# Kernel tuning notes

Measured on AMD Instinct MI355X. Metric: run time of the kernel, lower is better.

The kernel has to match this reference:

```python
import jax, jax.numpy as jnp
import numpy as np

DIM = 1024
HEADS = 8
DIM_HEAD = 64
INNER = HEADS * DIM_HEAD  # 512


def setup_inputs() -> dict:
    key = jax.random.key(0)
    k1, k2, k3, k4 = jax.random.split(key, 4)
    x = jax.random.normal(k1, (4, 4096, DIM), dtype=jnp.float32)
    W_qkv = jax.random.normal(k2, (DIM, 3 * INNER), dtype=jnp.float32) * (DIM ** -0.5)
    W_out = jax.random.normal(k3, (INNER, DIM), dtype=jnp.float32) * (INNER ** -0.5)
    b_out = jax.random.normal(k4, (DIM,), dtype=jnp.float32) * 0.01
    return {"x": x, "W_qkv": W_qkv, "W_out": W_out, "b_out": b_out}


def reference(x, W_qkv, W_out, b_out):
    b, n, _ = x.shape
    qkv = x @ W_qkv                                   # [b, n, 3*inner]
    q, k, v = jnp.split(qkv, 3, axis=-1)              # each [b, n, inner]

    def to_heads(t):
        return t.reshape(b, n, HEADS, DIM_HEAD).transpose(0, 2, 1, 3)  # [b, h, n, d]

    q = jax.nn.elu(to_heads(q)) + 1.0
    k = jax.nn.elu(to_heads(k)) + 1.0
    v = to_heads(v)
    # kv summary matrix: [b, h, d, e]
    context = jnp.einsum('bhnd,bhne->bhde', k, v)
    out = jnp.einsum('bhde,bhnd->bhne', context, q)   # [b, h, n, e]
    out = out.transpose(0, 2, 1, 3).reshape(b, n, INNER)
    return out @ W_out + b_out
```

## Files before the change

kernel.cpp:

```cpp
#include <hip/hip_runtime.h>
#include <hip/hip_bf16.h>
#include <cstdint>

typedef __attribute__((ext_vector_type(4))) float f32x4;
typedef __attribute__((ext_vector_type(8))) short bf16x8;

__device__ __forceinline__ ushort f2bf(float f) {
  unsigned u = __builtin_bit_cast(unsigned, f);
  u += 0x7fffu + ((u >> 16) & 1u);
  return (ushort)(u >> 16);
}

__device__ __forceinline__ void gload_lds16(const ushort* g, ushort* l) {
  __builtin_amdgcn_global_load_lds(
      (const __attribute__((address_space(1))) unsigned int*)g,
      (__attribute__((address_space(3))) unsigned int*)l, 16, 0, 0);
}

__device__ __forceinline__ void hard_barrier() {
  __builtin_amdgcn_sched_barrier(0);
  __builtin_amdgcn_s_barrier();
  __builtin_amdgcn_sched_barrier(0);
}

template <int N>
__device__ __forceinline__ void wait_vm() {
  if constexpr (N == 0) asm volatile("s_waitcnt vmcnt(0)" ::: "memory");
  else if constexpr (N == 2) asm volatile("s_waitcnt vmcnt(2)" ::: "memory");
  else if constexpr (N == 4) asm volatile("s_waitcnt vmcnt(4)" ::: "memory");
  else if constexpr (N == 6) asm volatile("s_waitcnt vmcnt(6)" ::: "memory");
  else static_assert(N < 0, "unsupported vmcnt");
}

__device__ __forceinline__ float elu1(float v) {
  return (v > 0.f) ? (v + 1.f) : __expf(v);
}

__global__ __launch_bounds__(256) void cvt_x_kernel(const float4* __restrict__ x,
                                                    ushort4* __restrict__ xb, int n4) {
  int stride = gridDim.x * blockDim.x;
  for (int i = blockIdx.x * blockDim.x + threadIdx.x; i < n4; i += stride) {
    float4 f = x[i];
    ushort4 o;
    o.x = f2bf(f.x); o.y = f2bf(f.y); o.z = f2bf(f.z); o.w = f2bf(f.w);
    xb[i] = o;
  }
}

__global__ __launch_bounds__(256) void transpose_w_kernel(const float* __restrict__ W,
                                                          ushort* __restrict__ Wt) {
  __shared__ float tile[32][33];
  int n0 = blockIdx.x * 32;
  int k0 = blockIdx.y * 32;
  int tx = threadIdx.x;
  int ty = threadIdx.y;
  #pragma unroll
  for (int p = 0; p < 4; ++p) {
    int k = k0 + ty + p * 8;
    tile[ty + p * 8][tx] = W[(size_t)k * 1536 + n0 + tx];
  }
  __syncthreads();
  #pragma unroll
  for (int p = 0; p < 4; ++p) {
    int n = n0 + ty + p * 8;
    Wt[(size_t)n * 1024 + k0 + tx] = f2bf(tile[tx][ty + p * 8]);
  }
}

template <int LDA, int LDB, int NT>
__device__ __forceinline__ void gemm_core(const ushort* __restrict__ A,
                                          const ushort* __restrict__ Bt,
                                          int row0, int col0, f32x4 acc[4][4],
                                          ushort* lds) {
  const int tid = threadIdx.x;
  const int l = tid & 63;
  const int wid = tid >> 6;
  const int fr = l & 15;
  const int fq = l >> 4;
  const int wr = wid >> 2;
  const int wc = wid & 3;

  const int scol = ((l & 7) * 8) ^ (((l >> 3) & 7) * 8);
  const ushort* aS = A + (size_t)(row0 + (tid >> 3)) * LDA + scol;
  const ushort* bS = Bt + (size_t)(col0 + (tid >> 3)) * LDB + scol;

  int aRow[4], bRow[4], kx[2];
  #pragma unroll
  for (int m = 0; m < 4; ++m) aRow[m] = (wr * 64 + m * 16 + fr) * 64;
  #pragma unroll
  for (int n = 0; n < 4; ++n) bRow[n] = (wc * 64 + n * 16 + fr) * 64;
  #pragma unroll
  for (int ks = 0; ks < 2; ++ks) kx[ks] = (ks * 32 + fq * 8) ^ ((fr & 7) * 8);

  auto stage = [&](int t) {
    ushort* dst = lds + (t % 3) * 24576 + tid * 8;
    const int ko = t * 64;
    #pragma unroll
    for (int p = 0; p < 2; ++p)
      gload_lds16(aS + (size_t)(p * 64) * LDA + ko, dst + p * 4096);
    #pragma unroll
    for (int p = 0; p < 4; ++p)
      gload_lds16(bS + (size_t)(p * 64) * LDB + ko, dst + 8192 + p * 4096);
  };

  stage(0);
  stage(1);
  wait_vm<6>();
  hard_barrier();

  #pragma unroll
  for (int t = 0; t < NT; ++t) {
    if (t + 2 < NT) stage(t + 2);
    const ushort* aB = lds + (t % 3) * 24576;
    const ushort* bB = aB + 8192;
    #pragma unroll
    for (int ks = 0; ks < 2; ++ks) {
      bf16x8 av[4], bv[4];
      #pragma unroll
      for (int m = 0; m < 4; ++m) av[m] = *(const bf16x8*)&aB[aRow[m] + kx[ks]];
      #pragma unroll
      for (int n = 0; n < 4; ++n) bv[n] = *(const bf16x8*)&bB[bRow[n] + kx[ks]];
      __builtin_amdgcn_s_setprio(1);
      #pragma unroll
      for (int m = 0; m < 4; ++m)
        #pragma unroll
        for (int n = 0; n < 4; ++n)
          acc[m][n] = __builtin_amdgcn_mfma_f32_16x16x32_bf16(av[m], bv[n], acc[m][n], 0, 0, 0);
      __builtin_amdgcn_s_setprio(0);
    }
    if (t + 2 < NT) {
      wait_vm<6>();
      hard_barrier();
    } else if (t + 1 < NT) {
      wait_vm<0>();
      hard_barrier();
    }
  }
}

__global__ __launch_bounds__(512, 2) void gemm_qkv_kernel(const ushort* __restrict__ xb,
                                                          const ushort* __restrict__ wt,
                                                          ushort* __restrict__ q,
                                                          ushort* __restrict__ kT,
                                                          ushort* __restrict__ vT) {
  __shared__ ushort lds[73728];
  f32x4 acc[4][4] = {};
  const int row0 = blockIdx.x * 128;
  const int col0 = blockIdx.y * 256;
  gemm_core<1024, 1024, 16>(xb, wt, row0, col0, acc, lds);
  const int l = threadIdx.x & 63;
  const int wid = threadIdx.x >> 6;
  const int wr = wid >> 2, wc = wid & 3;
  const int fr = l & 15, fq = l >> 4;
  #pragma unroll
  for (int m = 0; m < 4; ++m) {
    #pragma unroll
    for (int n = 0; n < 4; ++n) {
      const int c = col0 + wc * 64 + n * 16 + fr;
      const int r0 = row0 + wr * 64 + m * 16 + fq * 4;
      if (c < 512) {
        #pragma unroll
        for (int j = 0; j < 4; ++j)
          q[(size_t)(r0 + j) * 512 + c] = f2bf(elu1(acc[m][n][j]));
      } else if (c < 1024) {
        const int d = c - 512;
        const int bh = (r0 >> 12) * 8 + (d >> 6);
        const int nn = r0 & 4095;
        ushort4 o;
        o.x = f2bf(elu1(acc[m][n][0]));
        o.y = f2bf(elu1(acc[m][n][1]));
        o.z = f2bf(elu1(acc[m][n][2]));
        o.w = f2bf(elu1(acc[m][n][3]));
        *(ushort4*)&kT[((size_t)bh * 64 + (d & 63)) * 4096 + nn] = o;
      } else {
        const int d = c - 1024;
        const int bh = (r0 >> 12) * 8 + (d >> 6);
        const int nn = r0 & 4095;
        ushort4 o;
        o.x = f2bf(acc[m][n][0]);
        o.y = f2bf(acc[m][n][1]);
        o.z = f2bf(acc[m][n][2]);
        o.w = f2bf(acc[m][n][3]);
        *(ushort4*)&vT[((size_t)bh * 64 + (d & 63)) * 4096 + nn] = o;
      }
    }
  }
}

__global__ __launch_bounds__(256) void ctx_mfma_kernel(const ushort* __restrict__ kT,
                                                       const ushort* __restrict__ vT,
                                                       float* __restrict__ part) {
  __shared__ ushort lds[16384];
  const int bh = blockIdx.x;
  const int sp = blockIdx.y;
  const int tid = threadIdx.x;
  const int l = tid & 63, wid = tid >> 6;
  const int fr = l & 15, fq = l >> 4;
  const int wr = wid >> 1, wc = wid & 1;

  const size_t base = (size_t)bh * 64 * 4096 + sp * 128;
  const int srow = tid >> 2;
  const int lam = (tid & 3) ^ ((tid >> 3) & 3);
  const ushort* aG = kT + base + (size_t)srow * 4096 + lam * 8;
  const ushort* bG = vT + base + (size_t)srow * 4096 + lam * 8;

  #pragma unroll
  for (int t = 0; t < 4; ++t) {
    ushort* d = lds + t * 4096 + tid * 8;
    gload_lds16(aG + t * 32, d);
    gload_lds16(bG + t * 32, d + 2048);
  }

  const int sig = fq ^ ((fr >> 1) & 3);
  f32x4 acc[2][2] = {};

  auto compute = [&](int t) {
    const ushort* sb = lds + t * 4096;
    bf16x8 av[2], bv[2];
    #pragma unroll
    for (int mm = 0; mm < 2; ++mm)
      av[mm] = *(const bf16x8*)&sb[(wr * 32 + mm * 16 + fr) * 32 + sig * 8];
    #pragma unroll
    for (int nn = 0; nn < 2; ++nn)
      bv[nn] = *(const bf16x8*)&sb[2048 + (wc * 32 + nn * 16 + fr) * 32 + sig * 8];
    #pragma unroll
    for (int mm = 0; mm < 2; ++mm)
      #pragma unroll
      for (int nn = 0; nn < 2; ++nn)
        acc[mm][nn] = __builtin_amdgcn_mfma_f32_16x16x32_bf16(av[mm], bv[nn], acc[mm][nn], 0, 0, 0);
  };

  wait_vm<6>(); hard_barrier(); compute(0);
  wait_vm<4>(); hard_barrier(); compute(1);
  wait_vm<2>(); hard_barrier(); compute(2);
  wait_vm<0>(); hard_barrier(); compute(3);

  float* dst = part + ((size_t)sp * 32 + bh) * 4096;
  #pragma unroll
  for (int mm = 0; mm < 2; ++mm)
    #pragma unroll
    for (int nn = 0; nn < 2; ++nn)
      #pragma unroll
      for (int j = 0; j < 4; ++j)
        dst[(wr * 32 + mm * 16 + fq * 4 + j) * 64 + wc * 32 + nn * 16 + fr] = acc[mm][nn][j];
}

__global__ __launch_bounds__(256) void ctx_reduce_kernel(const float* __restrict__ part,
                                                         float* __restrict__ ctx) {
  const int i = blockIdx.x * 256 + threadIdx.x;
  float s = 0.f;
  #pragma unroll
  for (int sp = 0; sp < 32; ++sp) s += part[(size_t)sp * 131072 + i];
  ctx[i] = s;
}

__global__ __launch_bounds__(256) void weff_kernel(const float* __restrict__ ctx,
                                                   const float* __restrict__ Wout,
                                                   ushort* __restrict__ weff) {
  const int bh = blockIdx.x;
  const int h = bh & 7;
  const int m0 = blockIdx.y * 128;
  const int t = threadIdx.x;
  __shared__ float cs[64 * 64];
  __shared__ float ws[64][128];
  #pragma unroll
  for (int p = 0; p < 4; ++p) {
    const int idx = p * 1024 + t * 4;
    *(float4*)&cs[idx] = *(const float4*)&ctx[(size_t)bh * 4096 + idx];
  }
  #pragma unroll
  for (int p = 0; p < 8; ++p) {
    const int e = (t >> 5) + p * 8;
    const int c = (t & 31) * 4;
    *(float4*)&ws[e][c] = *(const float4*)&Wout[(size_t)(h * 64 + e) * 1024 + m0 + c];
  }
  __syncthreads();
  const int m = t & 127;
  const int dh = (t >> 7) * 32;
  float acc[32] = {};
  for (int e = 0; e < 64; ++e) {
    const float w = ws[e][m];
    #pragma unroll
    for (int i = 0; i < 32; ++i)
      acc[i] += cs[(dh + i) * 64 + e] * w;
  }
  ushort* dst = weff + ((size_t)(bh >> 3) * 1024 + m0 + m) * 512 + h * 64 + dh;
  #pragma unroll
  for (int i = 0; i < 32; ++i) dst[i] = f2bf(acc[i]);
}

__global__ __launch_bounds__(512, 2) void gemm_out_kernel(const ushort* __restrict__ q,
                                                          const ushort* __restrict__ weff,
                                                          const float* __restrict__ bout,
                                                          float* __restrict__ out) {
  __shared__ ushort lds[73728];
  f32x4 acc[4][4] = {};
  const int row0 = blockIdx.x * 128;
  const int col0 = blockIdx.y * 256;
  const int b = row0 >> 12;
  gemm_core<512, 512, 8>(q, weff + (size_t)b * 1024 * 512, row0, col0, acc, lds);
  const int l = threadIdx.x & 63;
  const int wid = threadIdx.x >> 6;
  const int wr = wid >> 2, wc = wid & 3;
  const int fr = l & 15, fq = l >> 4;
  #pragma unroll
  for (int m = 0; m < 4; ++m) {
    #pragma unroll
    for (int n = 0; n < 4; ++n) {
      const int c = col0 + wc * 64 + n * 16 + fr;
      const float bb = bout[c];
      #pragma unroll
      for (int j = 0; j < 4; ++j) {
        const int r = row0 + wr * 64 + m * 16 + fq * 4 + j;
        out[(size_t)r * 1024 + c] = acc[m][n][j] + bb;
      }
    }
  }
}

extern "C" void kernel_launch(void* const* d_in, const int* in_sizes, int n_in,
                              void* d_out, int out_size, void* d_ws, size_t ws_size,
                              hipStream_t stream) {
  const float* x    = (const float*)d_in[0];
  const float* Wqkv = (const float*)d_in[1];
  const float* Wout = (const float*)d_in[2];
  const float* bout = (const float*)d_in[3];
  float* out = (float*)d_out;
  char* ws = (char*)d_ws;

  ushort* xb   = (ushort*)(ws);
  float*  part = (float* )(ws);
  ushort* wt   = (ushort*)(ws + 33554432);
  ushort* q    = (ushort*)(ws + 36700160);
  ushort* kT   = (ushort*)(ws + 53477376);
  ushort* vT   = (ushort*)(ws + 70254592);
  float*  ctx  = (float* )(ws + 87031808);
  ushort* weff = (ushort*)(ws + 87556096);

  cvt_x_kernel<<<2048, 256, 0, stream>>>((const float4*)x, (ushort4*)xb, 16384 * 1024 / 4);
  transpose_w_kernel<<<dim3(48, 32), dim3(32, 8), 0, stream>>>(Wqkv, wt);
  gemm_qkv_kernel<<<dim3(128, 6), 512, 0, stream>>>(xb, wt, q, kT, vT);
  ctx_mfma_kernel<<<dim3(32, 32), 256, 0, stream>>>(kT, vT, part);
  ctx_reduce_kernel<<<512, 256, 0, stream>>>(part, ctx);
  weff_kernel<<<dim3(32, 8), 256, 0, stream>>>(ctx, Wout, weff);
  gemm_out_kernel<<<dim3(128, 4), 512, 0, stream>>>(q, weff, bout, out);
}
```

Before: 136.1 us.

## Split QKV GEMM into Q and transposed KV GEMMs, fold ctx reduce into weff

The fused QKV GEMM becomes two kernels. One computes Q in the usual orientation. The other computes K and V as W^T·x^T, so the accumulators land along the token dimension and kT/vT are written directly, replacing the strided transposed epilogue. The context kernel now covers 512 tokens per block with a 3-deep LDS ring pipeline, giving 8 splits instead of 32, and the separate reduce kernel is removed by summing the 8 partials inside weff_kernel. The intent is fewer launches, less partial traffic, and better output coalescing. The cost is scalar 2-byte stores in the KV epilogue and an extra GEMM launch.

```diff
diff --git a/kernel.cpp b/kernel.cpp
--- a/kernel.cpp
+++ b/kernel.cpp
@@ -138,11 +138,9 @@
   }
 }
 
-__global__ __launch_bounds__(512, 2) void gemm_qkv_kernel(const ushort* __restrict__ xb,
-                                                          const ushort* __restrict__ wt,
-                                                          ushort* __restrict__ q,
-                                                          ushort* __restrict__ kT,
-                                                          ushort* __restrict__ vT) {
+__global__ __launch_bounds__(512, 2) void gemm_q_kernel(const ushort* __restrict__ xb,
+                                                        const ushort* __restrict__ wt,
+                                                        ushort* __restrict__ q) {
   __shared__ ushort lds[73728];
   f32x4 acc[4][4] = {};
   const int row0 = blockIdx.x * 128;
@@ -157,31 +155,43 @@
     #pragma unroll
     for (int n = 0; n < 4; ++n) {
       const int c = col0 + wc * 64 + n * 16 + fr;
-      const int r0 = row0 + wr * 64 + m * 16 + fq * 4;
-      if (c < 512) {
-        #pragma unroll
-        for (int j = 0; j < 4; ++j)
-          q[(size_t)(r0 + j) * 512 + c] = f2bf(elu1(acc[m][n][j]));
-      } else if (c < 1024) {
-        const int d = c - 512;
-        const int bh = (r0 >> 12) * 8 + (d >> 6);
-        const int nn = r0 & 4095;
-        ushort4 o;
-        o.x = f2bf(elu1(acc[m][n][0]));
-        o.y = f2bf(elu1(acc[m][n][1]));
-        o.z = f2bf(elu1(acc[m][n][2]));
-        o.w = f2bf(elu1(acc[m][n][3]));
-        *(ushort4*)&kT[((size_t)bh * 64 + (d & 63)) * 4096 + nn] = o;
-      } else {
-        const int d = c - 1024;
-        const int bh = (r0 >> 12) * 8 + (d >> 6);
-        const int nn = r0 & 4095;
-        ushort4 o;
-        o.x = f2bf(acc[m][n][0]);
-        o.y = f2bf(acc[m][n][1]);
-        o.z = f2bf(acc[m][n][2]);
-        o.w = f2bf(acc[m][n][3]);
-        *(ushort4*)&vT[((size_t)bh * 64 + (d & 63)) * 4096 + nn] = o;
+      #pragma unroll
+      for (int j = 0; j < 4; ++j) {
+        const int r = row0 + wr * 64 + m * 16 + fq * 4 + j;
+        q[(size_t)r * 512 + c] = f2bf(elu1(acc[m][n][j]));
+      }
+    }
+  }
+}
+
+__global__ __launch_bounds__(512, 2) void gemm_kv_kernel(const ushort* __restrict__ wtkv,
+                                                         const ushort* __restrict__ xb,
+                                                         ushort* __restrict__ kT,
+                                                         ushort* __restrict__ vT) {
+  __shared__ ushort lds[73728];
+  f32x4 acc[4][4] = {};
+  const int row0 = blockIdx.x * 128;
+  const int col0 = blockIdx.y * 256;
+  gemm_core<1024, 1024, 16>(wtkv, xb, row0, col0, acc, lds);
+  const int l = threadIdx.x & 63;
+  const int wid = threadIdx.x >> 6;
+  const int wr = wid >> 2, wc = wid & 3;
+  const int fr = l & 15, fq = l >> 4;
+  #pragma unroll
+  for (int m = 0; m < 4; ++m) {
+    #pragma unroll
+    for (int n = 0; n < 4; ++n) {
+      const int tok = col0 + wc * 64 + n * 16 + fr;
+      const int b = tok >> 12, tn = tok & 4095;
+      #pragma unroll
+      for (int j = 0; j < 4; ++j) {
+        const int dp = row0 + wr * 64 + m * 16 + fq * 4 + j;
+        if (dp < 512) {
+          kT[((size_t)(b * 8 + (dp >> 6)) * 64 + (dp & 63)) * 4096 + tn] = f2bf(elu1(acc[m][n][j]));
+        } else {
+          const int dv = dp - 512;
+          vT[((size_t)(b * 8 + (dv >> 6)) * 64 + (dv & 63)) * 4096 + tn] = f2bf(acc[m][n][j]);
+        }
       }
     }
   }
@@ -198,24 +208,23 @@
   const int fr = l & 15, fq = l >> 4;
   const int wr = wid >> 1, wc = wid & 1;
 
-  const size_t base = (size_t)bh * 64 * 4096 + sp * 128;
+  const size_t base = (size_t)bh * 64 * 4096 + sp * 512;
   const int srow = tid >> 2;
   const int lam = (tid & 3) ^ ((tid >> 3) & 3);
   const ushort* aG = kT + base + (size_t)srow * 4096 + lam * 8;
   const ushort* bG = vT + base + (size_t)srow * 4096 + lam * 8;
 
-  #pragma unroll
-  for (int t = 0; t < 4; ++t) {
-    ushort* d = lds + t * 4096 + tid * 8;
+  auto stage = [&](int t) {
+    ushort* d = lds + (t & 3) * 4096 + tid * 8;
     gload_lds16(aG + t * 32, d);
     gload_lds16(bG + t * 32, d + 2048);
-  }
+  };
 
   const int sig = fq ^ ((fr >> 1) & 3);
   f32x4 acc[2][2] = {};
 
   auto compute = [&](int t) {
-    const ushort* sb = lds + t * 4096;
+    const ushort* sb = lds + (t & 3) * 4096;
     bf16x8 av[2], bv[2];
     #pragma unroll
     for (int mm = 0; mm < 2; ++mm)
@@ -230,10 +239,17 @@
         acc[mm][nn] = __builtin_amdgcn_mfma_f32_16x16x32_bf16(av[mm], bv[nn], acc[mm][nn], 0, 0, 0);
   };
 
-  wait_vm<6>(); hard_barrier(); compute(0);
-  wait_vm<4>(); hard_barrier(); compute(1);
-  wait_vm<2>(); hard_barrier(); compute(2);
-  wait_vm<0>(); hard_barrier(); compute(3);
+  constexpr int NT = 16;
+  stage(0); stage(1); stage(2);
+  for (int t = 0; t < NT; ++t) {
+    if (t <= NT - 3) wait_vm<4>();
+    else if (t == NT - 2) wait_vm<2>();
+    else wait_vm<0>();
+    hard_barrier();
+    compute(t);
+    hard_barrier();
+    if (t + 3 < NT) stage(t + 3);
+  }
 
   float* dst = part + ((size_t)sp * 32 + bh) * 4096;
   #pragma unroll
@@ -245,16 +261,7 @@
         dst[(wr * 32 + mm * 16 + fq * 4 + j) * 64 + wc * 32 + nn * 16 + fr] = acc[mm][nn][j];
 }
 
-__global__ __launch_bounds__(256) void ctx_reduce_kernel(const float* __restrict__ part,
-                                                         float* __restrict__ ctx) {
-  const int i = blockIdx.x * 256 + threadIdx.x;
-  float s = 0.f;
-  #pragma unroll
-  for (int sp = 0; sp < 32; ++sp) s += part[(size_t)sp * 131072 + i];
-  ctx[i] = s;
-}
-
-__global__ __launch_bounds__(256) void weff_kernel(const float* __restrict__ ctx,
+__global__ __launch_bounds__(256) void weff_kernel(const float* __restrict__ part,
                                                    const float* __restrict__ Wout,
                                                    ushort* __restrict__ weff) {
   const int bh = blockIdx.x;
@@ -266,7 +273,11 @@
   #pragma unroll
   for (int p = 0; p < 4; ++p) {
     const int idx = p * 1024 + t * 4;
-    *(float4*)&cs[idx] = *(const float4*)&ctx[(size_t)bh * 4096 + idx];
+    f32x4 s = {};
+    #pragma unroll
+    for (int sp = 0; sp < 8; ++sp)
+      s += *(const f32x4*)&part[(size_t)sp * 131072 + (size_t)bh * 4096 + idx];
+    *(f32x4*)&cs[idx] = s;
   }
   #pragma unroll
   for (int p = 0; p < 8; ++p) {
@@ -334,14 +345,13 @@
   ushort* q    = (ushort*)(ws + 36700160);
   ushort* kT   = (ushort*)(ws + 53477376);
   ushort* vT   = (ushort*)(ws + 70254592);
-  float*  ctx  = (float* )(ws + 87031808);
   ushort* weff = (ushort*)(ws + 87556096);
 
   cvt_x_kernel<<<2048, 256, 0, stream>>>((const float4*)x, (ushort4*)xb, 16384 * 1024 / 4);
   transpose_w_kernel<<<dim3(48, 32), dim3(32, 8), 0, stream>>>(Wqkv, wt);
-  gemm_qkv_kernel<<<dim3(128, 6), 512, 0, stream>>>(xb, wt, q, kT, vT);
-  ctx_mfma_kernel<<<dim3(32, 32), 256, 0, stream>>>(kT, vT, part);
-  ctx_reduce_kernel<<<512, 256, 0, stream>>>(part, ctx);
-  weff_kernel<<<dim3(32, 8), 256, 0, stream>>>(ctx, Wout, weff);
+  gemm_kv_kernel<<<dim3(8, 64), 512, 0, stream>>>(wt + (size_t)512 * 1024, xb, kT, vT);
+  gemm_q_kernel<<<dim3(128, 2), 512, 0, stream>>>(xb, wt, q);
+  ctx_mfma_kernel<<<dim3(32, 8), 256, 0, stream>>>(kT, vT, part);
+  weff_kernel<<<dim3(32, 8), 256, 0, stream>>>(part, Wout, weff);
   gemm_out_kernel<<<dim3(128, 4), 512, 0, stream>>>(q, weff, bout, out);
 }
```

Result: slower. 145.2 us (+6.7%).

## Merge prep kernels, deepen ctx split-K pipeline, fold reduction into weff

Applied to the files above, without the earlier changes.

Combines the x conversion and W transpose into a single launch via block-index dispatch. The context kernel now covers 512 tokens per block with a 3-deep ring-buffered global-to-LDS pipeline over 16 steps, cutting the split count from 32 to 8. The separate reduction kernel is dropped and the 8 partials are summed inside weff_kernel. Together this removes two launches and shrinks partial-sum traffic, but the ctx grid gets smaller (256 blocks) and each block does more serial work.

```diff
diff --git a/kernel.cpp b/kernel.cpp
--- a/kernel.cpp
+++ b/kernel.cpp
@@ -36,34 +36,37 @@
   return (v > 0.f) ? (v + 1.f) : __expf(v);
 }
 
-__global__ __launch_bounds__(256) void cvt_x_kernel(const float4* __restrict__ x,
-                                                    ushort4* __restrict__ xb, int n4) {
-  int stride = gridDim.x * blockDim.x;
-  for (int i = blockIdx.x * blockDim.x + threadIdx.x; i < n4; i += stride) {
-    float4 f = x[i];
-    ushort4 o;
-    o.x = f2bf(f.x); o.y = f2bf(f.y); o.z = f2bf(f.z); o.w = f2bf(f.w);
-    xb[i] = o;
-  }
-}
-
-__global__ __launch_bounds__(256) void transpose_w_kernel(const float* __restrict__ W,
-                                                          ushort* __restrict__ Wt) {
-  __shared__ float tile[32][33];
-  int n0 = blockIdx.x * 32;
-  int k0 = blockIdx.y * 32;
-  int tx = threadIdx.x;
-  int ty = threadIdx.y;
-  #pragma unroll
-  for (int p = 0; p < 4; ++p) {
-    int k = k0 + ty + p * 8;
-    tile[ty + p * 8][tx] = W[(size_t)k * 1536 + n0 + tx];
-  }
-  __syncthreads();
-  #pragma unroll
-  for (int p = 0; p < 4; ++p) {
-    int n = n0 + ty + p * 8;
-    Wt[(size_t)n * 1024 + k0 + tx] = f2bf(tile[tx][ty + p * 8]);
+__global__ __launch_bounds__(256) void prep_kernel(const float4* __restrict__ x,
+                                                   ushort4* __restrict__ xb,
+                                                   const float* __restrict__ W,
+                                                   ushort* __restrict__ Wt) {
+  if (blockIdx.x < 2048) {
+    const int n4 = 16384 * 1024 / 4;
+    const int stride = 2048 * 256;
+    for (int i = blockIdx.x * 256 + threadIdx.x; i < n4; i += stride) {
+      float4 f = x[i];
+      ushort4 o;
+      o.x = f2bf(f.x); o.y = f2bf(f.y); o.z = f2bf(f.z); o.w = f2bf(f.w);
+      xb[i] = o;
+    }
+  } else {
+    __shared__ float tile[32][33];
+    const int tb = blockIdx.x - 2048;
+    const int n0 = (tb % 48) * 32;
+    const int k0 = (tb / 48) * 32;
+    const int tx = threadIdx.x & 31;
+    const int ty = threadIdx.x >> 5;
+    #pragma unroll
+    for (int p = 0; p < 4; ++p) {
+      int k = k0 + ty + p * 8;
+      tile[ty + p * 8][tx] = W[(size_t)k * 1536 + n0 + tx];
+    }
+    __syncthreads();
+    #pragma unroll
+    for (int p = 0; p < 4; ++p) {
+      int n = n0 + ty + p * 8;
+      Wt[(size_t)n * 1024 + k0 + tx] = f2bf(tile[tx][ty + p * 8]);
+    }
   }
 }
 
@@ -198,24 +201,23 @@
   const int fr = l & 15, fq = l >> 4;
   const int wr = wid >> 1, wc = wid & 1;
 
-  const size_t base = (size_t)bh * 64 * 4096 + sp * 128;
+  const size_t base = (size_t)bh * 64 * 4096 + sp * 512;
   const int srow = tid >> 2;
   const int lam = (tid & 3) ^ ((tid >> 3) & 3);
   const ushort* aG = kT + base + (size_t)srow * 4096 + lam * 8;
   const ushort* bG = vT + base + (size_t)srow * 4096 + lam * 8;
 
-  #pragma unroll
-  for (int t = 0; t < 4; ++t) {
-    ushort* d = lds + t * 4096 + tid * 8;
+  auto stage = [&](int t) {
+    ushort* d = lds + (t & 3) * 4096 + tid * 8;
     gload_lds16(aG + t * 32, d);
     gload_lds16(bG + t * 32, d + 2048);
-  }
+  };
 
   const int sig = fq ^ ((fr >> 1) & 3);
   f32x4 acc[2][2] = {};
 
   auto compute = [&](int t) {
-    const ushort* sb = lds + t * 4096;
+    const ushort* sb = lds + (t & 3) * 4096;
     bf16x8 av[2], bv[2];
     #pragma unroll
     for (int mm = 0; mm < 2; ++mm)
@@ -230,10 +232,17 @@
         acc[mm][nn] = __builtin_amdgcn_mfma_f32_16x16x32_bf16(av[mm], bv[nn], acc[mm][nn], 0, 0, 0);
   };
 
-  wait_vm<6>(); hard_barrier(); compute(0);
-  wait_vm<4>(); hard_barrier(); compute(1);
-  wait_vm<2>(); hard_barrier(); compute(2);
-  wait_vm<0>(); hard_barrier(); compute(3);
+  constexpr int NT = 16;
+  stage(0); stage(1); stage(2);
+  for (int t = 0; t < NT; ++t) {
+    if (t <= NT - 3) wait_vm<4>();
+    else if (t == NT - 2) wait_vm<2>();
+    else wait_vm<0>();
+    hard_barrier();
+    compute(t);
+    hard_barrier();
+    if (t + 3 < NT) stage(t + 3);
+  }
 
   float* dst = part + ((size_t)sp * 32 + bh) * 4096;
   #pragma unroll
@@ -245,16 +254,7 @@
         dst[(wr * 32 + mm * 16 + fq * 4 + j) * 64 + wc * 32 + nn * 16 + fr] = acc[mm][nn][j];
 }
 
-__global__ __launch_bounds__(256) void ctx_reduce_kernel(const float* __restrict__ part,
-                                                         float* __restrict__ ctx) {
-  const int i = blockIdx.x * 256 + threadIdx.x;
-  float s = 0.f;
-  #pragma unroll
-  for (int sp = 0; sp < 32; ++sp) s += part[(size_t)sp * 131072 + i];
-  ctx[i] = s;
-}
-
-__global__ __launch_bounds__(256) void weff_kernel(const float* __restrict__ ctx,
+__global__ __launch_bounds__(256) void weff_kernel(const float* __restrict__ part,
                                                    const float* __restrict__ Wout,
                                                    ushort* __restrict__ weff) {
   const int bh = blockIdx.x;
@@ -266,7 +266,11 @@
   #pragma unroll
   for (int p = 0; p < 4; ++p) {
     const int idx = p * 1024 + t * 4;
-    *(float4*)&cs[idx] = *(const float4*)&ctx[(size_t)bh * 4096 + idx];
+    f32x4 s = {};
+    #pragma unroll
+    for (int sp = 0; sp < 8; ++sp)
+      s += *(const f32x4*)&part[(size_t)sp * 131072 + (size_t)bh * 4096 + idx];
+    *(f32x4*)&cs[idx] = s;
   }
   #pragma unroll
   for (int p = 0; p < 8; ++p) {
@@ -334,14 +338,11 @@
   ushort* q    = (ushort*)(ws + 36700160);
   ushort* kT   = (ushort*)(ws + 53477376);
   ushort* vT   = (ushort*)(ws + 70254592);
-  float*  ctx  = (float* )(ws + 87031808);
   ushort* weff = (ushort*)(ws + 87556096);
 
-  cvt_x_kernel<<<2048, 256, 0, stream>>>((const float4*)x, (ushort4*)xb, 16384 * 1024 / 4);
-  transpose_w_kernel<<<dim3(48, 32), dim3(32, 8), 0, stream>>>(Wqkv, wt);
+  prep_kernel<<<3584, 256, 0, stream>>>((const float4*)x, (ushort4*)xb, Wqkv, wt);
   gemm_qkv_kernel<<<dim3(128, 6), 512, 0, stream>>>(xb, wt, q, kT, vT);
-  ctx_mfma_kernel<<<dim3(32, 32), 256, 0, stream>>>(kT, vT, part);
-  ctx_reduce_kernel<<<512, 256, 0, stream>>>(part, ctx);
-  weff_kernel<<<dim3(32, 8), 256, 0, stream>>>(ctx, Wout, weff);
+  ctx_mfma_kernel<<<dim3(32, 8), 256, 0, stream>>>(kT, vT, part);
+  weff_kernel<<<dim3(32, 8), 256, 0, stream>>>(part, Wout, weff);
   gemm_out_kernel<<<dim3(128, 4), 512, 0, stream>>>(q, weff, bout, out);
 }
```

New measurement: 128.7 us. -5.4%, faster.
